# Kernel tuning notes

Hardware: AMD Instinct MI355X
Metric: run time of the kernel (lower is better)

## Reference

```python
import jax, jax.numpy as jnp
import numpy as np

B, H, V, NS, S, D, E = 4096, 256, 32000, 2, 128, 4, 64
PAD = 0


def _shift_matrices(n):
    # W_up: row i <- row i+1, last row zero. W_down: row i <- row i-1, row 0 zero.
    eye = np.eye(n, dtype=np.float32)
    W_up = np.vstack([eye[1:], np.zeros((1, n), np.float32)])
    W_down = np.vstack([np.zeros((1, n), np.float32), eye[:-1]])
    return W_up, W_down


def setup_inputs() -> dict:
    key = jax.random.key(0)
    ks = jax.random.split(key, 20)
    sc = 0.05
    emb_table = jax.random.normal(ks[0], (V, H), jnp.float32) * sc
    emb_table = emb_table.at[PAD].set(0.0)  # padding_idx
    inp = {
        "input_ids": jax.random.randint(ks[1], (B,), 0, V),
        "hidden": jax.random.normal(ks[2], (B, H), jnp.float32),
        "stacks": jax.random.normal(ks[3], (B, NS, S, E), jnp.float32),
        "emb_table": emb_table,
        "W_in": jax.random.normal(ks[4], (H, H), jnp.float32) * sc,
        "b_in": jnp.zeros((H,), jnp.float32),
        "W_hh": jax.random.normal(ks[5], (H, H), jnp.float32) * sc,
        "b_hh": jnp.zeros((H,), jnp.float32),
        "W_s2h": jax.random.normal(ks[6], (NS, H, D * E), jnp.float32) * sc,
        "b_s2h": jnp.zeros((NS, H), jnp.float32),
        "W_act": jax.random.normal(ks[7], (NS, 3, H), jnp.float32) * sc,
        "b_act": jnp.zeros((NS, 3), jnp.float32),
        "W_push": jax.random.normal(ks[8], (NS, E, H), jnp.float32) * sc,
        "b_push": jnp.zeros((NS, E), jnp.float32),
        "W_out": jax.random.normal(ks[9], (V, H), jnp.float32) * sc,
        "b_out": jnp.zeros((V,), jnp.float32),
        "empty_elem": jax.random.normal(ks[10], (1, E), jnp.float32),
    }
    return inp


def reference(input_ids, hidden, stacks, emb_table, W_in, b_in, W_hh, b_hh,
              W_s2h, b_s2h, W_act, b_act, W_push, b_push, W_out, b_out,
              empty_elem):
    W_up_np, W_down_np = _shift_matrices(S)
    W_up = jnp.asarray(W_up_np)
    W_down = jnp.asarray(W_down_np)

    emb = emb_table[input_ids]                                  # [B,H]
    mid = emb @ W_in.T + b_in + hidden @ W_hh.T + b_hh          # [B,H]

    # stack readout (top stack_depth elems), before any update
    stack_vals = stacks[:, :, :D, :].reshape(B, NS, D * E)      # [B,NS,D*E]
    mid = mid + jnp.einsum('bnd,nhd->bh', stack_vals, W_s2h) + b_s2h.sum(0)

    # per-stack actions from the OLD hidden state (no softmax in source)
    act = jnp.einsum('bh,nah->bna', hidden, W_act) + b_act      # [B,NS,3]
    p_push = act[..., 0:1]                                      # [B,NS,1]
    p_pop = act[..., 1:2]
    p_noop = act[..., 2:3]
    push_val = jnp.tanh(jnp.einsum('bh,neh->bne', hidden, W_push) + b_push)  # [B,NS,E]

    down = jnp.einsum('st,bnte->bnse', W_down, stacks)          # shift down
    up = jnp.einsum('st,bnte->bnse', W_up, stacks)              # shift up
    new_stacks = (p_push[..., None] * down + p_pop[..., None] * up
                  + p_noop[..., None] * stacks)
    new_stacks = new_stacks.at[:, :, 0, :].set(p_push * push_val)
    new_stacks = new_stacks.at[:, :, S - 1, :].set(
        jnp.broadcast_to(empty_elem[None], (B, NS, E)))

    new_hidden = jnp.tanh(mid)                                  # [B,H]
    logits = new_hidden @ W_out.T + b_out                       # [B,V]
    output = jax.nn.log_softmax(logits, axis=1)
    top1 = jnp.argmax(output, axis=1)[:, None]                  # [B,1]
    return output, new_hidden, top1, new_stacks
```

## Files before the change

kernel.cpp:

```cpp
#include <hip/hip_runtime.h>
#include <stdint.h>

#define B_   4096
#define H_   256
#define V_   32000
#define NS_  2
#define S_   128
#define E_   64
#define TRIG 0.02f
#define CSTR 10
#define NTV  125

typedef __attribute__((ext_vector_type(4))) float  f32x4;
typedef __attribute__((ext_vector_type(8))) __bf16 bf16x8;
typedef __attribute__((ext_vector_type(8))) unsigned short u16x8;

__device__ __forceinline__ unsigned short f2bf(float f) {
  unsigned u = __float_as_uint(f);
  u += 0x7fffu + ((u >> 16) & 1u);
  return (unsigned short)(u >> 16);
}

typedef __attribute__((address_space(1))) const unsigned int* gas1_t;
typedef __attribute__((address_space(3))) unsigned int*       las3_t;
__device__ __forceinline__ void gload16(const void* g, void* l) {
  __builtin_amdgcn_global_load_lds((gas1_t)g, (las3_t)l, 16, 0, 0);
}

__device__ __forceinline__ void merge2(float& m1, float& i1, float& m2, float& i2,
                                       float om1, float oi1, float om2, float oi2) {
  if (om1 > m1 || (om1 == m1 && oi1 < i1)) {
    const float lm = m1, li = i1;
    m1 = om1; i1 = oi1;
    if (lm > om2 || (lm == om2 && li < oi2)) { m2 = lm; i2 = li; }
    else { m2 = om2; i2 = oi2; }
  } else {
    if (om1 > m2 || (om1 == m2 && oi1 < i2)) { m2 = om1; i2 = oi1; }
  }
}

__global__ void prep_w1(const float* __restrict__ W_in,  const float* __restrict__ W_hh,
                        const float* __restrict__ W_s2h, const float* __restrict__ W_act,
                        const float* __restrict__ W_push,
                        const float* __restrict__ b_in,  const float* __restrict__ b_hh,
                        const float* __restrict__ b_s2h, const float* __restrict__ b_act,
                        const float* __restrict__ b_push,
                        unsigned short* __restrict__ W1, float* __restrict__ bbig) {
  const unsigned idx = blockIdx.x * 256u + threadIdx.x;
  const unsigned c = idx >> 10, k = idx & 1023u;
  float w = 0.f;
  if (c < 256u) {
    if (k < 256u)       w = W_in[c*256u + k];
    else if (k < 512u)  w = W_hh[c*256u + (k-256u)];
    else { unsigned n = (k-512u) >> 8, d = (k-512u) & 255u; w = W_s2h[n*65536u + c*256u + d]; }
  } else if (c < 262u) {
    if (k >= 256u && k < 512u) w = W_act[(c-256u)*256u + (k-256u)];
  } else if (c < 390u) {
    if (k >= 256u && k < 512u) w = W_push[(c-262u)*256u + (k-256u)];
  }
  W1[(size_t)c*1024u + k] = f2bf(w);
  if (idx < 512u) {
    float bb = 0.f;
    if (idx < 256u)       bb = b_in[idx] + b_hh[idx] + b_s2h[idx] + b_s2h[256u+idx];
    else if (idx < 262u)  bb = b_act[idx-256u];
    else if (idx < 390u)  bb = b_push[idx-262u];
    bbig[idx] = bb;
  }
}

__global__ void prep_w1t(const float* __restrict__ W_in, const float* __restrict__ W_hh,
                         const float* __restrict__ W_s2h, float* __restrict__ W1T) {
  const unsigned idx = blockIdx.x * 256u + threadIdx.x;
  const unsigned k = idx >> 8, h = idx & 255u;
  float w;
  if (k < 256u)      w = W_in[h*256u + k];
  else if (k < 512u) w = W_hh[h*256u + (k-256u)];
  else { unsigned n = (k-512u) >> 8, d = (k-512u) & 255u; w = W_s2h[n*65536u + h*256u + d]; }
  W1T[idx] = w;
}

__global__ void prep_a1(const int* __restrict__ ids, const float* __restrict__ emb,
                        const float* __restrict__ hidden, const float* __restrict__ stacks,
                        unsigned short* __restrict__ A1, float* __restrict__ A1f) {
  const unsigned gid = blockIdx.x * 256u + threadIdx.x;
  const unsigned b = gid >> 7, k0 = (gid & 127u) << 3;
  const float* src;
  if (k0 < 256u)      src = emb + (size_t)ids[b]*256u + k0;
  else if (k0 < 512u) src = hidden + (size_t)b*256u + (k0-256u);
  else { const unsigned kk = k0 - 512u;
         src = stacks + (size_t)b*16384u + (kk>>8)*8192u + (kk&255u); }
  const float4 v0 = *(const float4*)src;
  const float4 v1 = *(const float4*)(src + 4);
  *(float4*)(A1f + (size_t)b*1024u + k0)     = v0;
  *(float4*)(A1f + (size_t)b*1024u + k0 + 4) = v1;
  u16x8 o;
  o[0]=f2bf(v0.x); o[1]=f2bf(v0.y); o[2]=f2bf(v0.z); o[3]=f2bf(v0.w);
  o[4]=f2bf(v1.x); o[5]=f2bf(v1.y); o[6]=f2bf(v1.z); o[7]=f2bf(v1.w);
  *(u16x8*)(A1 + (size_t)b*1024u + k0) = o;
}

__global__ void prep_b2(const float* __restrict__ W_out, unsigned short* __restrict__ B2) {
  const unsigned gid = blockIdx.x * 256u + threadIdx.x;
  const size_t base = (size_t)gid * 8;
  const float4 v0 = *(const float4*)(W_out + base);
  const float4 v1 = *(const float4*)(W_out + base + 4);
  u16x8 o;
  o[0]=f2bf(v0.x); o[1]=f2bf(v0.y); o[2]=f2bf(v0.z); o[3]=f2bf(v0.w);
  o[4]=f2bf(v1.x); o[5]=f2bf(v1.y); o[6]=f2bf(v1.z); o[7]=f2bf(v1.w);
  *(u16x8*)(B2 + base) = o;
}

__global__ __launch_bounds__(256) void gemm_mid(
    const unsigned short* __restrict__ A, const unsigned short* __restrict__ Bm,
    float* __restrict__ nh_out, float* __restrict__ actw, float* __restrict__ pushw,
    const float* __restrict__ bbig, unsigned short* __restrict__ a2w)
{
  constexpr int K = 1024;
  constexpr int NT = K >> 6;
  __shared__ __align__(16) unsigned char pool[65536];
  const int tid  = threadIdx.x;
  const int lane = tid & 63;
  const int wid  = tid >> 6;
  const int wm = wid >> 1, wn = wid & 1;
  const int l16 = lane & 15;
  const int lk8 = (lane >> 4) << 3;
  const int lr4 = (lane >> 4) << 2;
  const size_t arow0 = (size_t)blockIdx.y << 7;
  const size_t bcol0 = (size_t)blockIdx.x << 7;

  f32x4 acc[4][4];
#pragma unroll
  for (int i = 0; i < 4; ++i)
#pragma unroll
    for (int j = 0; j < 4; ++j) acc[i][j] = (f32x4)0.f;

  auto stageAB = [&](int buf, int kt) {
    unsigned char* dst = pool + (buf << 15);
    const int k0 = kt << 6;
#pragma unroll
    for (int i = 0; i < 4; ++i) {
      const int e   = (i << 8) + tid;
      const int row = e >> 3;
      const int col = (e & 7) << 3;
      gload16(A  + (arow0 + row) * (size_t)K + (k0 + col), dst + (size_t)e * 16);
      gload16(Bm + (bcol0 + row) * (size_t)K + (k0 + col), dst + 16384 + (size_t)e * 16);
    }
  };
  auto computeT = [&](int buf) {
    const unsigned short* As = (const unsigned short*)(pool + (buf << 15));
    const unsigned short* Bs = As + 8192;
#pragma unroll
    for (int kk = 0; kk < 64; kk += 32) {
      bf16x8 af[4], bfr[4];
#pragma unroll
      for (int f = 0; f < 4; ++f) {
        af[f]  = *(const bf16x8*)&As[((wm<<6) + (f<<4) + l16)*64 + kk + lk8];
        bfr[f] = *(const bf16x8*)&Bs[((wn<<6) + (f<<4) + l16)*64 + kk + lk8];
      }
#pragma unroll
      for (int mf = 0; mf < 4; ++mf)
#pragma unroll
        for (int nf = 0; nf < 4; ++nf)
          acc[mf][nf] = __builtin_amdgcn_mfma_f32_16x16x32_bf16(af[mf], bfr[nf], acc[mf][nf], 0, 0, 0);
    }
  };

  stageAB(0, 0);
  stageAB(1, 1);
#pragma unroll
  for (int t = 0; t < NT; ++t) {
    if (t < NT - 1) asm volatile("s_waitcnt vmcnt(8)" ::: "memory");
    else            asm volatile("s_waitcnt vmcnt(0)" ::: "memory");
    __builtin_amdgcn_s_barrier();
    computeT(t & 1);
    __builtin_amdgcn_s_barrier();
    if (t + 2 < NT) stageAB(t & 1, t + 2);
  }

#pragma unroll
  for (int mf = 0; mf < 4; ++mf)
#pragma unroll
    for (int j = 0; j < 4; ++j) {
      const int r = (int)arow0 + (wm<<6) + (mf<<4) + lr4 + j;
#pragma unroll
      for (int nf = 0; nf < 4; ++nf) {
        const int c = (int)bcol0 + (wn<<6) + (nf<<4) + l16;
        const float v = acc[mf][nf][j] + bbig[c];
        if (c < 256) { const float th = tanhf(v);
                       nh_out[r*256 + c] = th;
                       a2w[r*256 + c] = f2bf(th); }
        else if (c < 262)  actw[r*6 + (c-256)] = v;
        else if (c < 390)  pushw[r*128 + (c-262)] = tanhf(v);
      }
    }
}

template<int MODE>
__global__ __launch_bounds__(512, 2) void gemm256(
    const unsigned short* __restrict__ Am, const unsigned short* __restrict__ Bn,
    float* __restrict__ gout, const float* __restrict__ b_out,
    float* __restrict__ partials, const float* __restrict__ subw)
{
  __shared__ __align__(16) unsigned char pool[131072];
  const int tid  = threadIdx.x;
  const int lane = tid & 63;
  const int wid  = tid >> 6;
  const int wm = wid >> 2;
  const int wn = wid & 3;
  const int l16 = lane & 15;
  const int g4  = lane >> 4;
  const int lr4 = g4 << 2;

  const int lin = ((int)blockIdx.x & 7) * 250 + ((int)blockIdx.x >> 3);
  const int bty = lin & 15;
  const int btx = lin >> 4;
  const size_t m0 = (size_t)(MODE == 0 ? bty : btx) << 8;
  const size_t n0 = (size_t)(MODE == 0 ? btx : bty) << 8;

  f32x4 acc[8][4];
#pragma unroll
  for (int m = 0; m < 8; ++m)
#pragma unroll
    for (int n = 0; n < 4; ++n) acc[m][n] = (f32x4)0.f;

  auto stage = [&](int buf, int ks) {
    unsigned char* da = pool + (buf ? 65536 : 0);
    unsigned char* db = da + 32768;
    const int k0 = ks << 6;
#pragma unroll
    for (int i = 0; i < 4; ++i) {
      const int e   = (i << 9) + tid;
      const int row = e >> 3;
      const int ch  = (e & 7) ^ (row & 7);
      gload16(Am + (m0 + row) * 256 + k0 + (ch << 3), da + (size_t)e * 16);
      gload16(Bn + (n0 + row) * 256 + k0 + (ch << 3), db + (size_t)e * 16);
    }
  };
  auto compute = [&](int buf) {
    const unsigned short* As = (const unsigned short*)(pool + (buf ? 65536 : 0));
    const unsigned short* Bs = As + 16384;
#pragma unroll
    for (int kk = 0; kk < 64; kk += 32) {
      const int cb = (kk >> 3) + g4;
      bf16x8 af[8], bfr[4];
#pragma unroll
      for (int m = 0; m < 8; ++m) {
        const int row = (wm<<7) + (m<<4) + l16;
        af[m] = *(const bf16x8*)&As[row*64 + ((cb ^ (row & 7)) << 3)];
      }
#pragma unroll
      for (int n = 0; n < 4; ++n) {
        const int row = (wn<<6) + (n<<4) + l16;
        bfr[n] = *(const bf16x8*)&Bs[row*64 + ((cb ^ (row & 7)) << 3)];
      }
#pragma unroll
      for (int m = 0; m < 8; ++m)
#pragma unroll
        for (int n = 0; n < 4; ++n)
          acc[m][n] = __builtin_amdgcn_mfma_f32_16x16x32_bf16(af[m], bfr[n], acc[m][n], 0, 0, 0);
    }
  };

  stage(0, 0);
  stage(1, 1);
#pragma unroll
  for (int t = 0; t < 4; ++t) {
    if (t < 3) asm volatile("s_waitcnt vmcnt(8)" ::: "memory");
    else       asm volatile("s_waitcnt vmcnt(0)" ::: "memory");
    __builtin_amdgcn_s_barrier();
    compute(t & 1);
    __builtin_amdgcn_s_barrier();
    if (t < 2) stage(t & 1, t + 2);
  }

  if constexpr (MODE == 0) {
    float* lf = (float*)pool;
#pragma unroll
    for (int ch = 0; ch < 4; ++ch) {
      __syncthreads();
      if (wm == (ch >> 1)) {
        const int mh = ch & 1;
#pragma unroll
        for (int mi = 0; mi < 4; ++mi) {
          const int m = mh*4 + mi;
#pragma unroll
          for (int n = 0; n < 4; ++n) {
            const int col = (wn<<6) + (n<<4) + l16;
#pragma unroll
            for (int j = 0; j < 4; ++j)
              lf[(mi*16 + lr4 + j)*260 + col] = acc[m][n][j];
          }
        }
      }
      __syncthreads();
      const int rbase = (ch >> 1)*128 + (ch & 1)*64;
#pragma unroll
      for (int it = 0; it < 8; ++it) {
        const int e  = (it << 9) + tid;
        const int r  = e >> 6;
        const int c4 = (e & 63) << 2;
        float4 v = *(float4*)&lf[r*260 + c4];
        const float4 bo4 = *(const float4*)&b_out[n0 + c4];
        const size_t grow = m0 + rbase + r;
        const float ls = subw[grow];
        v.x += bo4.x - ls; v.y += bo4.y - ls; v.z += bo4.z - ls; v.w += bo4.w - ls;
        *(float4*)&gout[grow * (size_t)V_ + n0 + c4] = v;
      }
    }
  } else {
    float (*colrec)[5] = (float (*)[5])&pool[0];
    float bo[32];
#pragma unroll
    for (int m = 0; m < 8; ++m)
#pragma unroll
      for (int j = 0; j < 4; ++j)
        bo[m*4+j] = b_out[m0 + (wm<<7) + (m<<4) + lr4 + j];

    float rS[4], rM1[4], rI1[4], rM2[4], rI2[4];
#pragma unroll
    for (int n = 0; n < 4; ++n) {
      float s = 0.f, m1 = -INFINITY, i1f = 2.1e9f, m2 = -INFINITY, i2f = 2.1e9f;
#pragma unroll
      for (int m = 0; m < 8; ++m)
#pragma unroll
        for (int j = 0; j < 4; ++j) {
          const int vloc = (wm<<7) + (m<<4) + lr4 + j;
          const float v = acc[m][n][j] + bo[m*4+j];
          const float fi = (float)((int)m0 + vloc);
          s += __expf(v);
          if (v > m1 || (v == m1 && fi < i1f)) { m2 = m1; i2f = i1f; m1 = v; i1f = fi; }
          else if (v > m2 || (v == m2 && fi < i2f)) { m2 = v; i2f = fi; }
        }
#pragma unroll
      for (int mask = 16; mask <= 32; mask <<= 1) {
        const float os  = __shfl_xor(s,   mask, 64);
        const float om1 = __shfl_xor(m1,  mask, 64);
        const float oi1 = __shfl_xor(i1f, mask, 64);
        const float om2 = __shfl_xor(m2,  mask, 64);
        const float oi2 = __shfl_xor(i2f, mask, 64);
        s += os;
        merge2(m1, i1f, m2, i2f, om1, oi1, om2, oi2);
      }
      rS[n] = s; rM1[n] = m1; rI1[n] = i1f; rM2[n] = m2; rI2[n] = i2f;
    }
    if (wm == 0 && g4 == 0) {
#pragma unroll
      for (int n = 0; n < 4; ++n) {
        const int cl = (wn<<6) + (n<<4) + l16;
        colrec[cl][0] = rS[n];  colrec[cl][1] = rM1[n]; colrec[cl][2] = rI1[n];
        colrec[cl][3] = rM2[n]; colrec[cl][4] = rI2[n];
      }
    }
    __syncthreads();
    if (wm == 1 && g4 == 0) {
#pragma unroll
      for (int n = 0; n < 4; ++n) {
        const int cl = (wn<<6) + (n<<4) + l16;
        float s = rS[n] + colrec[cl][0];
        float m1 = rM1[n], i1f = rI1[n], m2 = rM2[n], i2f = rI2[n];
        merge2(m1, i1f, m2, i2f, colrec[cl][1], colrec[cl][2], colrec[cl][3], colrec[cl][4]);
        const size_t brow = n0 + cl;
        float* dst = partials + (brow * NTV + btx) * 8;
        float4 v4; v4.x = s; v4.y = m1; v4.z = i1f; v4.w = m2;
        *(float4*)dst = v4;
        dst[4] = i2f;
      }
    }
  }
}

__global__ __launch_bounds__(256) void reduce_kernel(
    const float* __restrict__ partials, float* __restrict__ subw,
    float* __restrict__ top1w, int* __restrict__ candbuf)
{
  const int b = blockIdx.x, t = threadIdx.x;
  float s = 0.f, m1 = -INFINITY, i1 = 2.1e9f, m2 = -INFINITY, i2 = 2.1e9f;
  if (t < NTV) {
    const float4 p0 = *(const float4*)(partials + ((size_t)b*NTV + t)*8);
    s = p0.x; m1 = p0.y; i1 = p0.z; m2 = p0.w;
    i2 = partials[((size_t)b*NTV + t)*8 + 4];
  }
  __shared__ float sS[256], sM1[256], sI1[256], sM2[256], sI2[256];
  sS[t] = s; sM1[t] = m1; sI1[t] = i1; sM2[t] = m2; sI2[t] = i2;
  __syncthreads();
  for (int off = 128; off > 0; off >>= 1) {
    if (t < off) {
      sS[t] += sS[t+off];
      float a1 = sM1[t], ai1 = sI1[t], a2 = sM2[t], ai2 = sI2[t];
      merge2(a1, ai1, a2, ai2, sM1[t+off], sI1[t+off], sM2[t+off], sI2[t+off]);
      sM1[t] = a1; sI1[t] = ai1; sM2[t] = a2; sI2[t] = ai2;
    }
    __syncthreads();
  }
  const float M1 = sM1[0];
  __shared__ int cnt; __shared__ int cand[CSTR-1];
  if (t == 0) cnt = 0;
  __syncthreads();
  if (t < NTV) {
    if (m1 >= M1 - TRIG) { int p = atomicAdd(&cnt, 1); if (p < CSTR-1) cand[p] = (int)i1; }
    if (m2 >= M1 - TRIG) { int p = atomicAdd(&cnt, 1); if (p < CSTR-1) cand[p] = (int)i2; }
  }
  __syncthreads();
  const int ncand = min(cnt, CSTR-1);
  if (t == 0) {
    subw[b] = logf(sS[0]);
    candbuf[b*CSTR] = ncand;
    if (ncand <= 1) top1w[b] = sI1[0];
  }
  if (t < ncand) candbuf[b*CSTR + 1 + t] = cand[t];
}

__global__ __launch_bounds__(256) void rescue_kernel(
    const int* __restrict__ candbuf, const float* __restrict__ A1f,
    const float* __restrict__ W1T, const float* __restrict__ bbig,
    const float* __restrict__ W_out, const float* __restrict__ b_out,
    float* __restrict__ top1w)
{
  const int b = blockIdx.x;
  const int ncand = candbuf[b*CSTR];
  if (ncand <= 1) return;
  const int t = threadIdx.x;

  double acc = (double)bbig[t];
  const float* arow = A1f + (size_t)b * 1024;
  for (int k = 0; k < 1024; ++k)
    acc += (double)arow[k] * (double)W1T[k*256 + t];
  __shared__ double hbuf[256];
  hbuf[t] = tanh(acc);
  __syncthreads();

  __shared__ double red[256];
  double best = -1e300; int besti = 0x7fffffff;
  for (int q = 0; q < ncand; ++q) {
    const int ci = candbuf[b*CSTR + 1 + q];
    red[t] = hbuf[t] * (double)W_out[(size_t)ci*256 + t];
    __syncthreads();
    for (int off = 128; off > 0; off >>= 1) {
      if (t < off) red[t] += red[t+off];
      __syncthreads();
    }
    if (t == 0) {
      const double d = red[0] + (double)b_out[ci];
      if (d > best || (d == best && ci < besti)) { best = d; besti = ci; }
    }
    __syncthreads();
  }
  if (t == 0) top1w[b] = (float)besti;
}

__global__ void stacks_kernel(const float* __restrict__ stacks, const float* __restrict__ actw,
                              const float* __restrict__ pushw, const float* __restrict__ empty,
                              float* __restrict__ out3) {
  const int bn = blockIdx.x;
  const int b = bn >> 1, n = bn & 1;
  __shared__ __align__(16) float st[S_*E_];
  const float4* src4 = (const float4*)(stacks + (size_t)bn * (S_*E_));
  float4* st4 = (float4*)st;
  for (int i = threadIdx.x; i < (S_*E_/4); i += 256) st4[i] = src4[i];
  __syncthreads();
  const float pp = actw[b*6 + n*3 + 0];
  const float po = actw[b*6 + n*3 + 1];
  const float pq = actw[b*6 + n*3 + 2];
  float4* dst4 = (float4*)(out3 + (size_t)bn * (S_*E_));
  for (int i = threadIdx.x; i < (S_*E_/4); i += 256) {
    const int flat = i << 2;
    const int s = flat >> 6;
    const int e = flat & 63;
    float4 r;
    if (s == S_-1) {
      r = ((const float4*)empty)[e >> 2];
    } else if (s == 0) {
      const float4 pv = ((const float4*)(pushw + b*128 + n*64))[e >> 2];
      r.x = pp*pv.x; r.y = pp*pv.y; r.z = pp*pv.z; r.w = pp*pv.w;
    } else {
      const float4 dn = *(const float4*)&st[(s-1)*64 + e];
      const float4 up = *(const float4*)&st[(s+1)*64 + e];
      const float4 cu = *(const float4*)&st[s*64 + e];
      r.x = pp*dn.x + po*up.x + pq*cu.x;
      r.y = pp*dn.y + po*up.y + pq*cu.y;
      r.z = pp*dn.z + po*up.z + pq*cu.z;
      r.w = pp*dn.w + po*up.w + pq*cu.w;
    }
    dst4[i] = r;
  }
}

extern "C" void kernel_launch(void* const* d_in, const int* in_sizes, int n_in,
                              void* d_out, int out_size, void* d_ws, size_t ws_size,
                              hipStream_t stream) {
  (void)in_sizes; (void)n_in; (void)out_size; (void)ws_size;
  const int*   ids    = (const int*)  d_in[0];
  const float* hidden = (const float*)d_in[1];
  const float* stacks = (const float*)d_in[2];
  const float* emb    = (const float*)d_in[3];
  const float* W_in   = (const float*)d_in[4];
  const float* b_in   = (const float*)d_in[5];
  const float* W_hh   = (const float*)d_in[6];
  const float* b_hh   = (const float*)d_in[7];
  const float* W_s2h  = (const float*)d_in[8];
  const float* b_s2h  = (const float*)d_in[9];
  const float* W_act  = (const float*)d_in[10];
  const float* b_act  = (const float*)d_in[11];
  const float* W_push = (const float*)d_in[12];
  const float* b_push = (const float*)d_in[13];
  const float* W_out  = (const float*)d_in[14];
  const float* b_out  = (const float*)d_in[15];
  const float* empty  = (const float*)d_in[16];

  float* out0 = (float*)d_out;
  float* out1 = out0 + (size_t)B_*V_;
  float* out2 = out1 + (size_t)B_*H_;
  float* out3 = out2 + B_;

  unsigned short* A1 = (unsigned short*)out3;
  unsigned short* W1 = A1 + (size_t)4194304;
  unsigned short* A2 = W1 + (size_t)524288;
  unsigned short* B2 = A2 + (size_t)1048576;
  float* partials    = (float*)(B2 + (size_t)8192000);
  float* A1f         = partials + (size_t)8192000;
  float* W1T         = A1f + (size_t)4194304;
  int*   candbuf     = (int*)(W1T + 262144);

  float* bbig  = (float*)d_ws;
  float* actw  = bbig + 512;
  float* pushw = actw + (size_t)B_*6;
  float* subw  = pushw + (size_t)B_*128;

  prep_w1<<<dim3(2048),  dim3(256), 0, stream>>>(W_in, W_hh, W_s2h, W_act, W_push,
                                                 b_in, b_hh, b_s2h, b_act, b_push, W1, bbig);
  prep_w1t<<<dim3(1024), dim3(256), 0, stream>>>(W_in, W_hh, W_s2h, W1T);
  prep_a1<<<dim3(2048),  dim3(256), 0, stream>>>(ids, emb, hidden, stacks, A1, A1f);
  gemm_mid<<<dim3(4, 32), dim3(256), 0, stream>>>(A1, W1, out1, actw, pushw, bbig, A2);
  prep_b2<<<dim3(4000),  dim3(256), 0, stream>>>(W_out, B2);
  gemm256<2><<<dim3(2000), dim3(512), 0, stream>>>(B2, A2,
      nullptr, b_out, partials, nullptr);
  reduce_kernel<<<dim3(4096), dim3(256), 0, stream>>>(partials, subw, out2, candbuf);
  gemm256<0><<<dim3(2000), dim3(512), 0, stream>>>(A2, B2,
      out0, b_out, nullptr, subw);
  rescue_kernel<<<dim3(4096), dim3(256), 0, stream>>>(candbuf, A1f, W1T, bbig,
                                                      W_out, b_out, out2);
  stacks_kernel<<<dim3(8192), dim3(256), 0, stream>>>(stacks, actw, pushw, empty, out3);
}
```

Baseline: 637.6 us.

## Keep W_out tile resident in LDS and loop over batch tiles per block

Both vocab GEMMs are restructured so that each of 250 blocks loads a 128-row slice of W_out (bf16, full K=256) into LDS once. It then streams all 16 batch tiles of the hidden activations through a double-buffered pipeline, replacing 2000 independent 256x256 tiles. This removes repeated loads of the weight operand, and the partial-softmax layout doubles to 250 vocab tiles per row. The logits write switches to nontemporal stores. The cost is only 250 blocks at one block per CU with a serial batch loop and smaller per-wave tiles, which may underuse the GPU and hide latency less well.

```diff
diff --git a/kernel.cpp b/kernel.cpp
--- a/kernel.cpp
+++ b/kernel.cpp
@@ -9,7 +9,7 @@
 #define E_   64
 #define TRIG 0.02f
 #define CSTR 10
-#define NTV  125
+#define NTV  250
 
 typedef __attribute__((ext_vector_type(4))) float  f32x4;
 typedef __attribute__((ext_vector_type(8))) __bf16 bf16x8;
@@ -196,12 +196,13 @@
 }
 
 template<int MODE>
-__global__ __launch_bounds__(512, 2) void gemm256(
-    const unsigned short* __restrict__ Am, const unsigned short* __restrict__ Bn,
+__global__ __launch_bounds__(512, 1) void gemmBS(
+    const unsigned short* __restrict__ A2, const unsigned short* __restrict__ B2,
     float* __restrict__ gout, const float* __restrict__ b_out,
     float* __restrict__ partials, const float* __restrict__ subw)
 {
-  __shared__ __align__(16) unsigned char pool[131072];
+  __shared__ __align__(16) unsigned short Bres[128*256];
+  __shared__ __align__(16) unsigned short Apool[2][256*64];
   const int tid  = threadIdx.x;
   const int lane = tid & 63;
   const int wid  = tid >> 6;
@@ -210,161 +211,168 @@
   const int l16 = lane & 15;
   const int g4  = lane >> 4;
   const int lr4 = g4 << 2;
-
-  const int lin = ((int)blockIdx.x & 7) * 250 + ((int)blockIdx.x >> 3);
-  const int bty = lin & 15;
-  const int btx = lin >> 4;
-  const size_t m0 = (size_t)(MODE == 0 ? bty : btx) << 8;
-  const size_t n0 = (size_t)(MODE == 0 ? btx : bty) << 8;
-
-  f32x4 acc[8][4];
-#pragma unroll
-  for (int m = 0; m < 8; ++m)
-#pragma unroll
-    for (int n = 0; n < 4; ++n) acc[m][n] = (f32x4)0.f;
-
-  auto stage = [&](int buf, int ks) {
-    unsigned char* da = pool + (buf ? 65536 : 0);
-    unsigned char* db = da + 32768;
-    const int k0 = ks << 6;
+  const int vb  = (int)blockIdx.x << 7;
+
+  {
+#pragma unroll
+    for (int i = 0; i < 8; ++i) {
+      const int e   = (i << 9) + tid;
+      const int row = e >> 5;
+      const int c32 = e & 31;
+      const int src = (c32 & 24) | ((c32 ^ row) & 7);
+      gload16(B2 + (size_t)(vb + row) * 256 + (src << 3),
+              (unsigned char*)Bres + (size_t)e * 16);
+    }
+  }
+
+  auto stageA = [&](int buf, int bt, int kt) {
+    unsigned char* dst = (unsigned char*)Apool[buf];
 #pragma unroll
     for (int i = 0; i < 4; ++i) {
       const int e   = (i << 9) + tid;
       const int row = e >> 3;
-      const int ch  = (e & 7) ^ (row & 7);
-      gload16(Am + (m0 + row) * 256 + k0 + (ch << 3), da + (size_t)e * 16);
-      gload16(Bn + (n0 + row) * 256 + k0 + (ch << 3), db + (size_t)e * 16);
+      const int src = (e & 7) ^ (row & 7);
+      gload16(A2 + ((size_t)bt*256 + row) * 256 + kt*64 + (src << 3),
+              dst + (size_t)e * 16);
     }
   };
-  auto compute = [&](int buf) {
-    const unsigned short* As = (const unsigned short*)(pool + (buf ? 65536 : 0));
-    const unsigned short* Bs = As + 16384;
-#pragma unroll
-    for (int kk = 0; kk < 64; kk += 32) {
-      const int cb = (kk >> 3) + g4;
-      bf16x8 af[8], bfr[4];
-#pragma unroll
-      for (int m = 0; m < 8; ++m) {
-        const int row = (wm<<7) + (m<<4) + l16;
-        af[m] = *(const bf16x8*)&As[row*64 + ((cb ^ (row & 7)) << 3)];
-      }
+
+  for (int bt = 0; bt < 16; ++bt) {
+    f32x4 acc[4][4];
+#pragma unroll
+    for (int m = 0; m < 4; ++m)
+#pragma unroll
+      for (int n = 0; n < 4; ++n) acc[m][n] = (f32x4)0.f;
+
+    stageA(0, bt, 0);
+    stageA(1, bt, 1);
+#pragma unroll
+    for (int kt = 0; kt < 4; ++kt) {
+      if (kt < 3) asm volatile("s_waitcnt vmcnt(4)" ::: "memory");
+      else        asm volatile("s_waitcnt vmcnt(0)" ::: "memory");
+      __builtin_amdgcn_s_barrier();
+      const unsigned short* As = Apool[kt & 1];
+#pragma unroll
+      for (int kk = 0; kk < 64; kk += 32) {
+        bf16x8 af[4], bfr[4];
+#pragma unroll
+        for (int m = 0; m < 4; ++m) {
+          const int rb = (wm<<6) + (m<<4) + l16;
+          const int ch = kt*8 + (kk>>3) + g4;
+          const int s  = (ch & 24) | ((ch ^ rb) & 7);
+          af[m] = *(const bf16x8*)&Bres[rb*256 + (s<<3)];
+        }
+#pragma unroll
+        for (int n = 0; n < 4; ++n) {
+          const int ra = (wn<<6) + (n<<4) + l16;
+          const int s  = ((kk>>3) + g4) ^ (ra & 7);
+          bfr[n] = *(const bf16x8*)&As[ra*64 + (s<<3)];
+        }
+#pragma unroll
+        for (int m = 0; m < 4; ++m)
+#pragma unroll
+          for (int n = 0; n < 4; ++n)
+            acc[m][n] = __builtin_amdgcn_mfma_f32_16x16x32_bf16(af[m], bfr[n], acc[m][n], 0, 0, 0);
+      }
+      __builtin_amdgcn_s_barrier();
+      if (kt < 2) stageA(kt & 1, bt, kt + 2);
+    }
+
+    if constexpr (MODE == 0) {
+      float* lf = (float*)&Apool[0][0];
+#pragma unroll
+      for (int ch = 0; ch < 4; ++ch) {
+        __syncthreads();
+        if (wn == ch) {
+#pragma unroll
+          for (int m = 0; m < 4; ++m)
+#pragma unroll
+            for (int n = 0; n < 4; ++n) {
+              const int brow = (n<<4) + l16;
+              const int vcol = (wm<<6) + (m<<4) + lr4;
+#pragma unroll
+              for (int j = 0; j < 4; ++j)
+                lf[brow*129 + vcol + j] = acc[m][n][j];
+            }
+        }
+        __syncthreads();
+#pragma unroll
+        for (int it = 0; it < 4; ++it) {
+          const int idx = (it << 9) + tid;
+          const int r   = idx >> 5;
+          const int c4  = (idx & 31) << 2;
+          const size_t grow = (size_t)bt*256 + (ch<<6) + r;
+          const float ls = subw[grow];
+          f32x4 v;
+          v.x = lf[r*129 + c4 + 0] + b_out[vb + c4 + 0] - ls;
+          v.y = lf[r*129 + c4 + 1] + b_out[vb + c4 + 1] - ls;
+          v.z = lf[r*129 + c4 + 2] + b_out[vb + c4 + 2] - ls;
+          v.w = lf[r*129 + c4 + 3] + b_out[vb + c4 + 3] - ls;
+          __builtin_nontemporal_store(v, (f32x4*)(gout + grow * (size_t)V_ + vb + c4));
+        }
+      }
+      __syncthreads();
+    } else {
+      float (*colrec)[5] = (float (*)[5])&Apool[0][0];
+      float bo[16];
+#pragma unroll
+      for (int m = 0; m < 4; ++m)
+#pragma unroll
+        for (int j = 0; j < 4; ++j)
+          bo[m*4+j] = b_out[vb + (wm<<6) + (m<<4) + lr4 + j];
+
+      float rS[4], rM1[4], rI1[4], rM2[4], rI2[4];
 #pragma unroll
       for (int n = 0; n < 4; ++n) {
-        const int row = (wn<<6) + (n<<4) + l16;
-        bfr[n] = *(const bf16x8*)&Bs[row*64 + ((cb ^ (row & 7)) << 3)];
-      }
-#pragma unroll
-      for (int m = 0; m < 8; ++m)
-#pragma unroll
-        for (int n = 0; n < 4; ++n)
-          acc[m][n] = __builtin_amdgcn_mfma_f32_16x16x32_bf16(af[m], bfr[n], acc[m][n], 0, 0, 0);
-    }
-  };
-
-  stage(0, 0);
-  stage(1, 1);
-#pragma unroll
-  for (int t = 0; t < 4; ++t) {
-    if (t < 3) asm volatile("s_waitcnt vmcnt(8)" ::: "memory");
-    else       asm volatile("s_waitcnt vmcnt(0)" ::: "memory");
-    __builtin_amdgcn_s_barrier();
-    compute(t & 1);
-    __builtin_amdgcn_s_barrier();
-    if (t < 2) stage(t & 1, t + 2);
-  }
-
-  if constexpr (MODE == 0) {
-    float* lf = (float*)pool;
-#pragma unroll
-    for (int ch = 0; ch < 4; ++ch) {
+        float s = 0.f, m1 = -INFINITY, i1f = 2.1e9f, m2 = -INFINITY, i2f = 2.1e9f;
+#pragma unroll
+        for (int m = 0; m < 4; ++m)
+#pragma unroll
+          for (int j = 0; j < 4; ++j) {
+            const int vloc = (wm<<6) + (m<<4) + lr4 + j;
+            const float v = acc[m][n][j] + bo[m*4+j];
+            const float fi = (float)(vb + vloc);
+            s += __expf(v);
+            if (v > m1 || (v == m1 && fi < i1f)) { m2 = m1; i2f = i1f; m1 = v; i1f = fi; }
+            else if (v > m2 || (v == m2 && fi < i2f)) { m2 = v; i2f = fi; }
+          }
+#pragma unroll
+        for (int mask = 16; mask <= 32; mask <<= 1) {
+          const float os  = __shfl_xor(s,   mask, 64);
+          const float om1 = __shfl_xor(m1,  mask, 64);
+          const float oi1 = __shfl_xor(i1f, mask, 64);
+          const float om2 = __shfl_xor(m2,  mask, 64);
+          const float oi2 = __shfl_xor(i2f, mask, 64);
+          s += os;
+          merge2(m1, i1f, m2, i2f, om1, oi1, om2, oi2);
+        }
+        rS[n] = s; rM1[n] = m1; rI1[n] = i1f; rM2[n] = m2; rI2[n] = i2f;
+      }
       __syncthreads();
-      if (wm == (ch >> 1)) {
-        const int mh = ch & 1;
-#pragma unroll
-        for (int mi = 0; mi < 4; ++mi) {
-          const int m = mh*4 + mi;
-#pragma unroll
-          for (int n = 0; n < 4; ++n) {
-            const int col = (wn<<6) + (n<<4) + l16;
-#pragma unroll
-            for (int j = 0; j < 4; ++j)
-              lf[(mi*16 + lr4 + j)*260 + col] = acc[m][n][j];
-          }
+      if (wm == 0 && g4 == 0) {
+#pragma unroll
+        for (int n = 0; n < 4; ++n) {
+          const int cl = (wn<<6) + (n<<4) + l16;
+          colrec[cl][0] = rS[n];  colrec[cl][1] = rM1[n]; colrec[cl][2] = rI1[n];
+          colrec[cl][3] = rM2[n]; colrec[cl][4] = rI2[n];
         }
       }
       __syncthreads();
-      const int rbase = (ch >> 1)*128 + (ch & 1)*64;
-#pragma unroll
-      for (int it = 0; it < 8; ++it) {
-        const int e  = (it << 9) + tid;
-        const int r  = e >> 6;
-        const int c4 = (e & 63) << 2;
-        float4 v = *(float4*)&lf[r*260 + c4];
-        const float4 bo4 = *(const float4*)&b_out[n0 + c4];
-        const size_t grow = m0 + rbase + r;
-        const float ls = subw[grow];
-        v.x += bo4.x - ls; v.y += bo4.y - ls; v.z += bo4.z - ls; v.w += bo4.w - ls;
-        *(float4*)&gout[grow * (size_t)V_ + n0 + c4] = v;
-      }
-    }
-  } else {
-    float (*colrec)[5] = (float (*)[5])&pool[0];
-    float bo[32];
-#pragma unroll
-    for (int m = 0; m < 8; ++m)
-#pragma unroll
-      for (int j = 0; j < 4; ++j)
-        bo[m*4+j] = b_out[m0 + (wm<<7) + (m<<4) + lr4 + j];
-
-    float rS[4], rM1[4], rI1[4], rM2[4], rI2[4];
-#pragma unroll
-    for (int n = 0; n < 4; ++n) {
-      float s = 0.f, m1 = -INFINITY, i1f = 2.1e9f, m2 = -INFINITY, i2f = 2.1e9f;
-#pragma unroll
-      for (int m = 0; m < 8; ++m)
-#pragma unroll
-        for (int j = 0; j < 4; ++j) {
-          const int vloc = (wm<<7) + (m<<4) + lr4 + j;
-          const float v = acc[m][n][j] + bo[m*4+j];
-          const float fi = (float)((int)m0 + vloc);
-          s += __expf(v);
-          if (v > m1 || (v == m1 && fi < i1f)) { m2 = m1; i2f = i1f; m1 = v; i1f = fi; }
-          else if (v > m2 || (v == m2 && fi < i2f)) { m2 = v; i2f = fi; }
-        }
-#pragma unroll
-      for (int mask = 16; mask <= 32; mask <<= 1) {
-        const float os  = __shfl_xor(s,   mask, 64);
-        const float om1 = __shfl_xor(m1,  mask, 64);
-        const float oi1 = __shfl_xor(i1f, mask, 64);
-        const float om2 = __shfl_xor(m2,  mask, 64);
-        const float oi2 = __shfl_xor(i2f, mask, 64);
-        s += os;
-        merge2(m1, i1f, m2, i2f, om1, oi1, om2, oi2);
-      }
-      rS[n] = s; rM1[n] = m1; rI1[n] = i1f; rM2[n] = m2; rI2[n] = i2f;
-    }
-    if (wm == 0 && g4 == 0) {
-#pragma unroll
-      for (int n = 0; n < 4; ++n) {
-        const int cl = (wn<<6) + (n<<4) + l16;
-        colrec[cl][0] = rS[n];  colrec[cl][1] = rM1[n]; colrec[cl][2] = rI1[n];
-        colrec[cl][3] = rM2[n]; colrec[cl][4] = rI2[n];
-      }
-    }
-    __syncthreads();
-    if (wm == 1 && g4 == 0) {
-#pragma unroll
-      for (int n = 0; n < 4; ++n) {
-        const int cl = (wn<<6) + (n<<4) + l16;
-        float s = rS[n] + colrec[cl][0];
-        float m1 = rM1[n], i1f = rI1[n], m2 = rM2[n], i2f = rI2[n];
-        merge2(m1, i1f, m2, i2f, colrec[cl][1], colrec[cl][2], colrec[cl][3], colrec[cl][4]);
-        const size_t brow = n0 + cl;
-        float* dst = partials + (brow * NTV + btx) * 8;
-        float4 v4; v4.x = s; v4.y = m1; v4.z = i1f; v4.w = m2;
-        *(float4*)dst = v4;
-        dst[4] = i2f;
-      }
+      if (wm == 1 && g4 == 0) {
+#pragma unroll
+        for (int n = 0; n < 4; ++n) {
+          const int cl = (wn<<6) + (n<<4) + l16;
+          float s = rS[n] + colrec[cl][0];
+          float m1 = rM1[n], i1f = rI1[n], m2 = rM2[n], i2f = rI2[n];
+          merge2(m1, i1f, m2, i2f, colrec[cl][1], colrec[cl][2], colrec[cl][3], colrec[cl][4]);
+          const size_t brow = (size_t)bt*256 + cl;
+          float* dst = partials + (brow * NTV + blockIdx.x) * 8;
+          float4 v4; v4.x = s; v4.y = m1; v4.z = i1f; v4.w = m2;
+          *(float4*)dst = v4;
+          dst[4] = i2f;
+        }
+      }
+      __syncthreads();
     }
   }
 }
@@ -532,10 +540,10 @@
   prep_a1<<<dim3(2048),  dim3(256), 0, stream>>>(ids, emb, hidden, stacks, A1, A1f);
   gemm_mid<<<dim3(4, 32), dim3(256), 0, stream>>>(A1, W1, out1, actw, pushw, bbig, A2);
   prep_b2<<<dim3(4000),  dim3(256), 0, stream>>>(W_out, B2);
-  gemm256<2><<<dim3(2000), dim3(512), 0, stream>>>(B2, A2,
+  gemmBS<2><<<dim3(250), dim3(512), 0, stream>>>(A2, B2,
       nullptr, b_out, partials, nullptr);
   reduce_kernel<<<dim3(4096), dim3(256), 0, stream>>>(partials, subw, out2, candbuf);
-  gemm256<0><<<dim3(2000), dim3(512), 0, stream>>>(A2, B2,
+  gemmBS<0><<<dim3(250), dim3(512), 0, stream>>>(A2, B2,
       out0, b_out, nullptr, subw);
   rescue_kernel<<<dim3(4096), dim3(256), 0, stream>>>(candbuf, A1f, W1T, bbig,
                                                       W_out, b_out, out2);
```

Result: faster. 577.9 us (-9.4%).
